# Kernel tuning notes

Hardware: AMD Instinct MI355X
Metric: run time of the kernel (lower is better)

The kernel has to match this reference:

```python
import jax, jax.numpy as jnp
import numpy as np

T, B = 2048, 128
H = 128          # hidden_size
QH = 1024        # query_hidden_size
NF = 32          # num_convolution_filters
K = 31           # convolution_filter_size (odd, same padding)


def setup_inputs() -> dict:
    key = jax.random.key(0)
    ks = jax.random.split(key, 10)
    encoded_tokens = jax.random.normal(ks[0], (T, B, H), dtype=jnp.float32)
    tokens_mask = jax.random.randint(ks[1], (B, T), 0, 2).astype(jnp.bool_)
    query = jax.random.normal(ks[2], (1, B, QH), dtype=jnp.float32)
    cumulative_alignment = jax.random.uniform(ks[3], (B, T), dtype=jnp.float32)
    # parameters
    conv_w = jax.random.normal(ks[4], (NF, 1, K), dtype=jnp.float32) * 0.1   # Conv1d weight [out,in,k]
    conv_b = jnp.zeros((NF,), dtype=jnp.float32)
    Wq = jax.random.normal(ks[5], (H, QH), dtype=jnp.float32) * (1.0 / np.sqrt(QH))
    bq = jnp.zeros((H,), dtype=jnp.float32)
    Wa = jax.random.normal(ks[6], (H, NF), dtype=jnp.float32) * (1.0 / np.sqrt(NF))
    ba = jnp.zeros((H,), dtype=jnp.float32)
    score_w = jax.random.normal(ks[7], (H,), dtype=jnp.float32) * (1.0 / np.sqrt(H))  # xavier-ish
    score_b = jnp.zeros((H,), dtype=jnp.float32)
    return dict(encoded_tokens=encoded_tokens, tokens_mask=tokens_mask, query=query,
                cumulative_alignment=cumulative_alignment, conv_w=conv_w, conv_b=conv_b,
                Wq=Wq, bq=bq, Wa=Wa, ba=ba, score_w=score_w, score_b=score_b)


def reference(encoded_tokens, tokens_mask, query, cumulative_alignment,
              conv_w, conv_b, Wq, bq, Wa, ba, score_w, score_b):
    # location features: Conv1d over cumulative alignment, same padding
    loc = jax.lax.conv_general_dilated(
        cumulative_alignment[:, None, :], conv_w,
        window_strides=(1,), padding=[((K - 1) // 2, (K - 1) // 2)],
        dimension_numbers=('NCH', 'OIH', 'NCH'))  # [B, NF, T]
    loc = loc + conv_b[None, :, None]
    loc = jnp.transpose(loc, (2, 0, 1))                        # [T, B, NF]
    loc = jnp.einsum('tbf,hf->tbh', loc, Wa) + ba              # [T, B, H]
    q = jnp.einsum('obq,hq->obh', query, Wq) + bq              # [1, B, H]
    # additive score: tanh of fused elementwise sum, then project to scalar
    score = jnp.tanh(encoded_tokens + q + loc + score_b)       # [T, B, H]
    s = jnp.einsum('tbh,h->bt', score, score_w)                # [B, T]
    s = jnp.where(tokens_mask, -jnp.inf, s)
    alignment = jax.nn.softmax(s, axis=1)                      # [B, T]
    context = jnp.einsum('bt,tbh->bh', alignment, encoded_tokens)  # [B, H]
    cumulative_alignment = cumulative_alignment + alignment
    return context, cumulative_alignment, alignment
```

## Files before the change

kernel.cpp:

```cpp
#include <hip/hip_runtime.h>
#include <stdint.h>

#define T_DIM 2048
#define B_DIM 128
#define H_DIM 128
#define QH_DIM 1024
#define NF 32
#define KW 31
#define TB 128
#define NTILE (T_DIM / TB)
#define CPAD_ROW (T_DIM + 32)

#define PREP_NB 512
#define G_NB 8

#define NEG_INF (-__builtin_inff())

typedef float v2f __attribute__((ext_vector_type(2)));

__device__ __forceinline__ float fast_tanh(float x) {
    float e = __expf(2.0f * x);
    return 1.0f - 2.0f * __builtin_amdgcn_rcpf(1.0f + e);
}

template <int C>
__device__ __forceinline__ float dpp_add(float x) {
    int m = __builtin_amdgcn_update_dpp(0, __float_as_int(x), C, 0xf, 0xf, true);
    return x + __int_as_float(m);
}
__device__ __forceinline__ float wave_sum64(float x) {
    x = dpp_add<0x111>(x); x = dpp_add<0x112>(x); x = dpp_add<0x114>(x); x = dpp_add<0x118>(x);
    x = dpp_add<0x142>(x); x = dpp_add<0x143>(x);
    return __int_as_float(__builtin_amdgcn_readlane(__float_as_int(x), 63));
}

__global__ __launch_bounds__(512)
void kA_prep(const float* __restrict__ cum, const void* __restrict__ mask,
             float* __restrict__ cpad, float* __restrict__ mbias,
             const float* __restrict__ Wa, const float* __restrict__ conv_w,
             float* __restrict__ Gt,
             const float* __restrict__ query, const float* __restrict__ Wq,
             const float* __restrict__ bq, const float* __restrict__ conv_b,
             const float* __restrict__ ba, const float* __restrict__ score_b,
             float* __restrict__ qb) {
    const int bid = blockIdx.x;
    const int tid = threadIdx.x;

    if (bid < PREP_NB) {
        const int gid = bid * 512 + tid;
        const int b = gid >> 11, t = gid & 2047;
        const int l = tid & 63;
        uint32_t u = ((const uint32_t*)mask)[l];
        unsigned long long hi = __ballot(u > 1u);
        unsigned long long nf = __ballot(u != 0u && u != 0x3f800000u);
        int layout = (hi == 0ull) ? 0 : ((nf == 0ull) ? 2 : 1);
        bool m;
        if (layout == 0)      m = ((const int32_t*)mask)[gid] != 0;
        else if (layout == 1) m = ((const uint8_t*)mask)[gid] != 0;
        else                  m = ((const float*)mask)[gid] != 0.0f;
        mbias[gid] = m ? NEG_INF : 0.0f;
        cpad[b * CPAD_ROW + 16 + t] = cum[gid];
        if (t < 16) cpad[b * CPAD_ROW + t] = 0.0f;
        else if (t >= T_DIM - 16) cpad[b * CPAD_ROW + 32 + t] = 0.0f;
    } else if (bid < PREP_NB + G_NB) {
        const int gid = (bid - PREP_NB) * 512 + tid;
        if (gid < KW * H_DIM) {
            const int k = gid >> 7, h = gid & 127;
            float acc = 0.0f;
            #pragma unroll
            for (int f = 0; f < NF; ++f) acc = fmaf(Wa[h * NF + f], conv_w[f * KW + k], acc);
            Gt[gid] = acc;
        }
    } else {
        const int b = bid - (PREP_NB + G_NB);
        const int h = tid & 127, qtr = tid >> 7;
        __shared__ __align__(16) float qrow[QH_DIM];
        __shared__ float partial[512];
        for (int i = tid; i < QH_DIM; i += 512) qrow[i] = query[b * QH_DIM + i];
        __syncthreads();
        const float4* wq4 = (const float4*)(Wq + (size_t)h * QH_DIM + qtr * 256);
        const float4* q4 = (const float4*)(qrow + qtr * 256);
        float acc = 0.0f;
        #pragma unroll 4
        for (int j = 0; j < 64; ++j) {
            float4 w = wq4[j], q = q4[j];
            acc += w.x * q.x + w.y * q.y + w.z * q.z + w.w * q.w;
        }
        if (qtr == 0) {
            float cb = bq[h] + ba[h] + score_b[h];
            #pragma unroll
            for (int f = 0; f < NF; ++f) cb = fmaf(Wa[h * NF + f], conv_b[f], cb);
            acc += cb;
        }
        partial[tid] = acc;
        __syncthreads();
        if (tid < 128)
            qb[b * H_DIM + h] = partial[h] + partial[h + 128] + partial[h + 256] + partial[h + 384];
    }
}

__global__ __launch_bounds__(256, 2)
void k2_fused(const float* __restrict__ enc, const float* __restrict__ cpad,
              const float* __restrict__ mbias, const float* __restrict__ Gt,
              const float* __restrict__ qb, const float* __restrict__ score_w,
              float* __restrict__ s_out, float* __restrict__ o_part,
              float* __restrict__ ml_part) {
    const int b = blockIdx.x;
    const int tl = blockIdx.y;
    const int tid = threadIdx.x;
    const int l = tid & 63;
    const int wv = __builtin_amdgcn_readfirstlane(tid >> 6);
    const int tw0 = tl * TB + wv * 32;

    __shared__ float oc[4][H_DIM];
    __shared__ float mwl[4], lwl[4];

    v2f G[KW];
    #pragma unroll
    for (int k = 0; k < KW; ++k) G[k] = *(const v2f*)(Gt + k * H_DIM + 2 * l);

    const v2f base = *(const v2f*)(qb + b * H_DIM + 2 * l);
    const v2f w2 = *(const v2f*)(score_w + 2 * l);
    const float* crow = cpad + b * CPAD_ROW;
    const float* mrow = mbias + b * T_DIM;

    float m_w = NEG_INF, l_w = 0.0f;
    v2f o = {0.0f, 0.0f};
    float sv = 0.0f;

    #pragma unroll
    for (int c = 0; c < 4; ++c) {
        const int tb = tw0 + c * 8;

        float sc[38];
        #pragma unroll
        for (int j = 0; j < 38; ++j) sc[j] = crow[tb + 1 + j];

        v2f ee[8];
        #pragma unroll
        for (int it = 0; it < 8; ++it)
            ee[it] = *(const v2f*)(enc + ((size_t)(tb + it) * B_DIM + b) * H_DIM + 2 * l);

        float su[8];
        #pragma unroll
        for (int it = 0; it < 8; ++it) {
            v2f acc = base;
            #pragma unroll
            for (int k = 0; k < KW; ++k)
                acc = __builtin_elementwise_fma(G[k], (v2f){sc[it + k], sc[it + k]}, acc);
            const v2f a2 = acc + ee[it];
            float p = w2.x * fast_tanh(a2.x) + w2.y * fast_tanh(a2.y);
            su[it] = wave_sum64(p) + mrow[tb + it];
        }

        #pragma unroll
        for (int it = 0; it < 8; ++it) sv = (l == c * 8 + it) ? su[it] : sv;

        float m8 = su[0];
        #pragma unroll
        for (int it = 1; it < 8; ++it) m8 = fmaxf(m8, su[it]);
        const float m_new = fmaxf(m_w, m8);
        const float m_use = (m_new == NEG_INF) ? 0.0f : m_new;
        const float alpha = __expf(m_w - m_use);
        float lsum = 0.0f;
        v2f osum = {0.0f, 0.0f};
        #pragma unroll
        for (int it = 0; it < 8; ++it) {
            const float e = __expf(su[it] - m_use);
            lsum += e;
            osum = __builtin_elementwise_fma((v2f){e, e}, ee[it], osum);
        }
        l_w = fmaf(l_w, alpha, lsum);
        o = __builtin_elementwise_fma(o, (v2f){alpha, alpha}, osum);
        m_w = m_new;
    }

    if (l < 32) s_out[b * T_DIM + tw0 + l] = sv;

    oc[wv][2 * l] = o.x;
    oc[wv][2 * l + 1] = o.y;
    if (l == 0) { mwl[wv] = m_w; lwl[wv] = l_w; }
    __syncthreads();
    if (tid < H_DIM) {
        const float mb = fmaxf(fmaxf(mwl[0], mwl[1]), fmaxf(mwl[2], mwl[3]));
        const float mu = (mb == NEG_INF) ? 0.0f : mb;
        const float b0 = __expf(mwl[0] - mu), b1 = __expf(mwl[1] - mu);
        const float b2 = __expf(mwl[2] - mu), b3 = __expf(mwl[3] - mu);
        const float ov = oc[0][tid] * b0 + oc[1][tid] * b1 + oc[2][tid] * b2 + oc[3][tid] * b3;
        const int tbase = b * NTILE + tl;
        o_part[tbase * H_DIM + tid] = ov;
        if (tid == 0) {
            ml_part[tbase * 2] = mb;
            ml_part[tbase * 2 + 1] = lwl[0] * b0 + lwl[1] * b1 + lwl[2] * b2 + lwl[3] * b3;
        }
    }
}

__global__ __launch_bounds__(256)
void k5_final(float* __restrict__ s_align, const float* __restrict__ cum_in,
              float* __restrict__ cum_out, const float* __restrict__ o_part,
              const float* __restrict__ ml_part, float* __restrict__ ctx) {
    const int b = blockIdx.x, tid = threadIdx.x;
    __shared__ float sm[NTILE], sl[NTILE], sb[NTILE];
    if (tid < NTILE) {
        sm[tid] = ml_part[(b * NTILE + tid) * 2];
        sl[tid] = ml_part[(b * NTILE + tid) * 2 + 1];
    }
    __syncthreads();
    float M = sm[0];
    #pragma unroll
    for (int i = 1; i < NTILE; ++i) M = fmaxf(M, sm[i]);
    const float M_use = (M == NEG_INF) ? 0.0f : M;
    if (tid < NTILE) sb[tid] = __expf(sm[tid] - M_use);
    __syncthreads();
    float L = 0.0f;
    #pragma unroll
    for (int i = 0; i < NTILE; ++i) L = fmaf(sl[i], sb[i], L);
    const float invL = 1.0f / L;
    if (tid < H_DIM) {
        float ov = 0.0f;
        #pragma unroll
        for (int i = 0; i < NTILE; ++i)
            ov = fmaf(o_part[(b * NTILE + i) * H_DIM + tid], sb[i], ov);
        ctx[b * H_DIM + tid] = ov * invL;
    }
    #pragma unroll
    for (int j = 0; j < 8; ++j) {
        const int idx = b * T_DIM + tid + j * 256;
        const float a = __expf(s_align[idx] - M_use) * invL;
        s_align[idx] = a;
        cum_out[idx] = cum_in[idx] + a;
    }
}

extern "C" void kernel_launch(void* const* d_in, const int* in_sizes, int n_in,
                              void* d_out, int out_size, void* d_ws, size_t ws_size,
                              hipStream_t stream) {
    const float* enc     = (const float*)d_in[0];
    const void*  mask    = d_in[1];
    const float* query   = (const float*)d_in[2];
    const float* cum     = (const float*)d_in[3];
    const float* conv_w  = (const float*)d_in[4];
    const float* conv_b  = (const float*)d_in[5];
    const float* Wq      = (const float*)d_in[6];
    const float* bq      = (const float*)d_in[7];
    const float* Wa      = (const float*)d_in[8];
    const float* ba      = (const float*)d_in[9];
    const float* score_w = (const float*)d_in[10];
    const float* score_b = (const float*)d_in[11];

    float* ctx_out   = (float*)d_out;
    float* cum_out   = ctx_out + B_DIM * H_DIM;
    float* align_out = cum_out + B_DIM * T_DIM;

    float* Gt     = (float*)d_ws;
    float* qb     = Gt + 4096;
    float* o_part = qb + B_DIM * H_DIM;
    float* ml     = o_part + B_DIM * NTILE * H_DIM;
    float* cpad   = ml + 8192;
    float* mb     = cpad + B_DIM * CPAD_ROW;

    kA_prep<<<PREP_NB + G_NB + B_DIM, 512, 0, stream>>>(
        cum, mask, cpad, mb, Wa, conv_w, Gt,
        query, Wq, bq, conv_b, ba, score_b, qb);
    k2_fused<<<dim3(B_DIM, NTILE), 256, 0, stream>>>(enc, cpad, mb, Gt, qb, score_w,
                                                     align_out, o_part, ml);
    k5_final<<<B_DIM, 256, 0, stream>>>(align_out, cum, cum_out, o_part, ml, ctx_out);
}
```

Baseline: 237.1 us.

## Double-buffer encoder loads, hoist conv window, raise occupancy, split final kernel

The fused score kernel now loads all 62 cumulative-alignment values and 32 mask biases once per wave. It also double-buffers the encoder rows, prefetching the next 8-timestep chunk while the current one is computed, and raises the launch-bounds occupancy hint from 2 to 3 blocks per SIMD. The final normalization kernel is split across 4 segments per batch row for more parallelism. The larger register footprint combined with the tighter occupancy bound risks register spills.

```diff
diff --git a/kernel.cpp b/kernel.cpp
--- a/kernel.cpp
+++ b/kernel.cpp
@@ -99,7 +99,7 @@
     }
 }
 
-__global__ __launch_bounds__(256, 2)
+__global__ __launch_bounds__(256, 3)
 void k2_fused(const float* __restrict__ enc, const float* __restrict__ cpad,
               const float* __restrict__ mbias, const float* __restrict__ Gt,
               const float* __restrict__ qb, const float* __restrict__ score_w,
@@ -123,23 +123,34 @@
     const v2f w2 = *(const v2f*)(score_w + 2 * l);
     const float* crow = cpad + b * CPAD_ROW;
     const float* mrow = mbias + b * T_DIM;
+    const float* erow = enc + (size_t)tw0 * B_DIM * H_DIM + (size_t)b * H_DIM + 2 * l;
+
+    float sc[62];
+    #pragma unroll
+    for (int j = 0; j < 62; ++j) sc[j] = crow[tw0 + 1 + j];
+    float mr[32];
+    #pragma unroll
+    for (int j = 0; j < 32; ++j) mr[j] = mrow[tw0 + j];
 
     float m_w = NEG_INF, l_w = 0.0f;
     v2f o = {0.0f, 0.0f};
     float sv = 0.0f;
 
+    v2f eeb[2][8];
+    #pragma unroll
+    for (int it = 0; it < 8; ++it)
+        eeb[0][it] = *(const v2f*)(erow + (size_t)it * B_DIM * H_DIM);
+
     #pragma unroll
     for (int c = 0; c < 4; ++c) {
-        const int tb = tw0 + c * 8;
-
-        float sc[38];
-        #pragma unroll
-        for (int j = 0; j < 38; ++j) sc[j] = crow[tb + 1 + j];
-
-        v2f ee[8];
-        #pragma unroll
-        for (int it = 0; it < 8; ++it)
-            ee[it] = *(const v2f*)(enc + ((size_t)(tb + it) * B_DIM + b) * H_DIM + 2 * l);
+        const int tb = c * 8;
+
+        if (c < 3) {
+            #pragma unroll
+            for (int it = 0; it < 8; ++it)
+                eeb[(c + 1) & 1][it] =
+                    *(const v2f*)(erow + (size_t)(tb + 8 + it) * B_DIM * H_DIM);
+        }
 
         float su[8];
         #pragma unroll
@@ -147,14 +158,14 @@
             v2f acc = base;
             #pragma unroll
             for (int k = 0; k < KW; ++k)
-                acc = __builtin_elementwise_fma(G[k], (v2f){sc[it + k], sc[it + k]}, acc);
-            const v2f a2 = acc + ee[it];
+                acc = __builtin_elementwise_fma(G[k], (v2f){sc[tb + it + k], sc[tb + it + k]}, acc);
+            const v2f a2 = acc + eeb[c & 1][it];
             float p = w2.x * fast_tanh(a2.x) + w2.y * fast_tanh(a2.y);
-            su[it] = wave_sum64(p) + mrow[tb + it];
-        }
-
-        #pragma unroll
-        for (int it = 0; it < 8; ++it) sv = (l == c * 8 + it) ? su[it] : sv;
+            su[it] = wave_sum64(p) + mr[tb + it];
+        }
+
+        #pragma unroll
+        for (int it = 0; it < 8; ++it) sv = (l == tb + it) ? su[it] : sv;
 
         float m8 = su[0];
         #pragma unroll
@@ -168,7 +179,7 @@
         for (int it = 0; it < 8; ++it) {
             const float e = __expf(su[it] - m_use);
             lsum += e;
-            osum = __builtin_elementwise_fma((v2f){e, e}, ee[it], osum);
+            osum = __builtin_elementwise_fma((v2f){e, e}, eeb[c & 1][it], osum);
         }
         l_w = fmaf(l_w, alpha, lsum);
         o = __builtin_elementwise_fma(o, (v2f){alpha, alpha}, osum);
@@ -200,7 +211,7 @@
 void k5_final(float* __restrict__ s_align, const float* __restrict__ cum_in,
               float* __restrict__ cum_out, const float* __restrict__ o_part,
               const float* __restrict__ ml_part, float* __restrict__ ctx) {
-    const int b = blockIdx.x, tid = threadIdx.x;
+    const int b = blockIdx.x, seg = blockIdx.y, tid = threadIdx.x;
     __shared__ float sm[NTILE], sl[NTILE], sb[NTILE];
     if (tid < NTILE) {
         sm[tid] = ml_part[(b * NTILE + tid) * 2];
@@ -217,7 +228,7 @@
     #pragma unroll
     for (int i = 0; i < NTILE; ++i) L = fmaf(sl[i], sb[i], L);
     const float invL = 1.0f / L;
-    if (tid < H_DIM) {
+    if (seg == 0 && tid < H_DIM) {
         float ov = 0.0f;
         #pragma unroll
         for (int i = 0; i < NTILE; ++i)
@@ -225,8 +236,8 @@
         ctx[b * H_DIM + tid] = ov * invL;
     }
     #pragma unroll
-    for (int j = 0; j < 8; ++j) {
-        const int idx = b * T_DIM + tid + j * 256;
+    for (int j = 0; j < 2; ++j) {
+        const int idx = b * T_DIM + seg * 512 + tid + j * 256;
         const float a = __expf(s_align[idx] - M_use) * invL;
         s_align[idx] = a;
         cum_out[idx] = cum_in[idx] + a;
@@ -265,5 +276,5 @@
         query, Wq, bq, conv_b, ba, score_b, qb);
     k2_fused<<<dim3(B_DIM, NTILE), 256, 0, stream>>>(enc, cpad, mb, Gt, qb, score_w,
                                                      align_out, o_part, ml);
-    k5_final<<<B_DIM, 256, 0, stream>>>(align_out, cum, cum_out, o_part, ml, ctx_out);
-}
+    k5_final<<<dim3(B_DIM, 4), 256, 0, stream>>>(align_out, cum, cum_out, o_part, ml, ctx_out);
+}
```

Result: no change. 239.0 us (+0.8%).
